# Kernel optimization log

Measured on AMD Instinct MI355X. Metric: run time of the kernel, lower is better.

## Reference

```python
import jax, jax.numpy as jnp
import numpy as np

T, B, IN, H, L = 300, 32, 320, 1024, 3  # seq, batch, input, hidden, layers (bidirectional)


def _init_params(key):
    stdv = 1.0 / np.sqrt(H)
    ks = jax.random.split(key, 8)
    u = lambda k, shp: jax.random.uniform(k, shp, jnp.float32, -stdv, stdv)
    # layer 0 (input IN), 2 directions
    w_ih0 = u(ks[0], (2, 4 * H, IN))
    w_hh0 = u(ks[1], (2, 4 * H, H))
    b_ih0 = u(ks[2], (2, 4 * H))
    b_hh0 = u(ks[3], (2, 4 * H))
    # layers 1..L-1 (input 2H), 2 directions
    w_ihL = u(ks[4], (L - 1, 2, 4 * H, 2 * H))
    w_hhL = u(ks[5], (L - 1, 2, 4 * H, H))
    b_ihL = u(ks[6], (L - 1, 2, 4 * H))
    b_hhL = u(ks[7], (L - 1, 2, 4 * H))
    # forget_gate_bias = 1.0 applied to bias_ih[H:2H], bias_hh[H:2H] = 0
    fgb = 1.0
    b_ih0 = b_ih0.at[:, H:2 * H].set(fgb)
    b_hh0 = b_hh0.at[:, H:2 * H].set(0.0)
    b_ihL = b_ihL.at[:, :, H:2 * H].set(fgb)
    b_hhL = b_hhL.at[:, :, H:2 * H].set(0.0)
    return dict(w_ih0=w_ih0, w_hh0=w_hh0, b_ih0=b_ih0, b_hh0=b_hh0,
                w_ihL=w_ihL, w_hhL=w_hhL, b_ihL=b_ihL, b_hhL=b_hhL)


def setup_inputs() -> dict:
    key = jax.random.key(0)
    k1, k2 = jax.random.split(key)
    inp = {
        "x": jax.random.normal(k1, (T, B, IN), jnp.float32),
        "h0": jnp.zeros((L * 2, B, H), jnp.float32),
        "c0": jnp.zeros((L * 2, B, H), jnp.float32),
    }
    inp.update(_init_params(k2))
    return inp


def _hard_sigmoid(z):
    return jnp.clip(0.2 * z + 0.5, 0.0, 1.0)


def _lstm_dir(x_seq, w_ih, w_hh, b_ih, b_hh, h0, c0, reverse):
    # x_seq: [T, B, D_in]; returns ys [T,B,H], (h,c) [B,H]
    xs = jnp.flip(x_seq, 0) if reverse else x_seq
    gx = jnp.einsum('tbi,gi->tbg', xs, w_ih) + b_ih + b_hh  # [T,B,4H]

    def step(carry, gxt):
        h, c = carry
        gates = gxt + h @ w_hh.T
        i, f, g, o = jnp.split(gates, 4, axis=-1)
        i = _hard_sigmoid(i)
        f = _hard_sigmoid(f)
        g = jnp.clip(g, -1.0, 1.0)  # hardtanh
        o = _hard_sigmoid(o)
        c = f * c + i * g
        h = o * jnp.clip(c, -1.0, 1.0)
        return (h, c), h

    (h, c), ys = jax.lax.scan(step, (h0, c0), gx)
    if reverse:
        ys = jnp.flip(ys, 0)
    return ys, h, c


def _stacked_forward(x, h0, c0, w_ih0, w_hh0, b_ih0, b_hh0, w_ihL, w_hhL, b_ihL, b_hhL):
    # Faithful to StackedLSTM: hn = hx[0].view(L,2,B,H); cn = hn (source bug: cell
    # init comes from h0, c0 ignored). h0/c0 are zeros so this is also correct math.
    hn = h0.reshape(L, 2, B, H)
    cn = hn
    out = x
    hs, cs = [], []
    for l in range(L):
        if l == 0:
            wih, whh, bih, bhh = w_ih0, w_hh0, b_ih0, b_hh0
        else:
            wih, whh, bih, bhh = w_ihL[l - 1], w_hhL[l - 1], b_ihL[l - 1], b_hhL[l - 1]
        yf, hf, cf = _lstm_dir(out, wih[0], whh[0], bih[0], bhh[0], hn[l, 0], cn[l, 0], False)
        yb, hb, cb = _lstm_dir(out, wih[1], whh[1], bih[1], bhh[1], hn[l, 1], cn[l, 1], True)
        out = jnp.concatenate([yf, yb], axis=-1)  # [T,B,2H]
        hs += [hf, hb]
        cs += [cf, cb]
    hn_out = jnp.stack(hs)  # [L*2, B, H]
    cn_out = jnp.stack(cs)
    return out, hn_out, cn_out


def reference(x, h0, c0, w_ih0, w_hh0, b_ih0, b_hh0, w_ihL, w_hhL, b_ihL, b_hhL):
    return _stacked_forward(x, h0, c0, w_ih0, w_hh0, b_ih0, b_hh0,
                            w_ihL, w_hhL, b_ihL, b_hhL)
```

## Files before the change

kernel.cpp:

```cpp
#include <hip/hip_runtime.h>

typedef __bf16 bf16;
typedef __attribute__((ext_vector_type(8))) __bf16 bf16x8;
typedef __attribute__((ext_vector_type(4))) float f32x4;

#define GLOBAL_AS __attribute__((address_space(1)))
#define LDS_AS __attribute__((address_space(3)))

__device__ __forceinline__ void gload_lds16(const void* g, void* l) {
  __builtin_amdgcn_global_load_lds((const GLOBAL_AS void*)g, (LDS_AS void*)l, 16, 0, 0);
}
__device__ __forceinline__ void gload_lds16_sc0(const void* g, void* l) {
  __builtin_amdgcn_global_load_lds((const GLOBAL_AS void*)g, (LDS_AS void*)l, 16, 0, 0x1);
}

__device__ __forceinline__ f32x4 mfma16(bf16x8 a, bf16x8 b, f32x4 c) {
  return __builtin_amdgcn_mfma_f32_16x16x32_bf16(a, b, c, 0, 0, 0);
}

#define GBAR() asm volatile("s_barrier" ::: "memory")

#define T_SEQ 300
#define NBATCH 32
#define DIN 320
#define NH 1024
#define NG 4096
#define MROWS 9600
#define OUT_Y 19660800
#define HN_SZ 196608
#define FPAD 32
#define ELEC_A (64 * FPAD)
#define ELEC_B (64 * FPAD + 8)
#define ELEC_R0 (64 * FPAD + 16)
#define ELEC_R1 (64 * FPAD + 24)
#define ELEC_G (64 * FPAD + 32)

__global__ __launch_bounds__(256) void k_cvt(const float* __restrict__ src,
                                             bf16* __restrict__ dst, int n8) {
  int stride = gridDim.x * blockDim.x;
  for (int i = blockIdx.x * blockDim.x + threadIdx.x; i < n8; i += stride) {
    const float* s = src + (size_t)i * 8;
    f32x4 a = *(const f32x4*)s;
    f32x4 b = *(const f32x4*)(s + 4);
    bf16x8 o;
#pragma unroll
    for (int j = 0; j < 4; ++j) { o[j] = (bf16)a[j]; o[j + 4] = (bf16)b[j]; }
    *(bf16x8*)(dst + (size_t)i * 8) = o;
  }
}

__global__ __launch_bounds__(256) void k_bsum(const float* __restrict__ bih0,
                                              const float* __restrict__ bhh0,
                                              const float* __restrict__ bihL,
                                              const float* __restrict__ bhhL,
                                              float* __restrict__ bsum) {
  int i = blockIdx.x * 256 + threadIdx.x;
  if (i < 2 * NG) bsum[i] = bih0[i] + bhh0[i];
  else            bsum[i] = bihL[i - 2 * NG] + bhhL[i - 2 * NG];
}

__global__ __launch_bounds__(256) void k_gemm_gx(const bf16* __restrict__ A,
                                                 const bf16* __restrict__ Bw,
                                                 const float* __restrict__ bias,
                                                 bf16* __restrict__ gxout, int K) {
  __shared__ bf16 As[128 * 32];
  __shared__ bf16 Bs[128 * 32];
  const int t = threadIdx.x;
  const int m0 = blockIdx.y * 128, n0 = blockIdx.x * 128;
  const int lane = t & 63, wid = t >> 6;
  const int wr = wid >> 1, wc = wid & 1;
  const int fr = lane & 15, fq = lane >> 4;
  f32x4 acc[4][4] = {};
  for (int k0 = 0; k0 < K; k0 += 32) {
#pragma unroll
    for (int r = 0; r < 2; ++r) {
      int idx = r * 256 + t;
      int row = idx >> 2, kk = (idx & 3) * 8;
      gload_lds16(A + (size_t)(m0 + row) * K + k0 + kk, As + (size_t)idx * 8);
      gload_lds16(Bw + (size_t)(n0 + row) * K + k0 + kk, Bs + (size_t)idx * 8);
    }
    asm volatile("s_waitcnt vmcnt(0)" ::: "memory");
    __syncthreads();
    bf16x8 af[4], bf_[4];
#pragma unroll
    for (int i2 = 0; i2 < 4; ++i2) {
      af[i2]  = *(const bf16x8*)(As + (wr * 64 + i2 * 16 + fr) * 32 + fq * 8);
      bf_[i2] = *(const bf16x8*)(Bs + (wc * 64 + i2 * 16 + fr) * 32 + fq * 8);
    }
#pragma unroll
    for (int mi = 0; mi < 4; ++mi)
#pragma unroll
      for (int ni = 0; ni < 4; ++ni)
        acc[mi][ni] = mfma16(af[mi], bf_[ni], acc[mi][ni]);
    __syncthreads();
  }
#pragma unroll
  for (int ni = 0; ni < 4; ++ni) {
    int col = n0 + wc * 64 + ni * 16 + fr;
    float bv = bias[col];
    int dir = col >> 12, grow = col & (NG - 1);
    int gg = grow >> 10, uu = grow & 1023;
    bf16* base = gxout + ((size_t)dir * 300 * 4 + gg) * 32768 + uu;
#pragma unroll
    for (int mi = 0; mi < 4; ++mi) {
#pragma unroll
      for (int j = 0; j < 4; ++j) {
        int row = m0 + wr * 64 + mi * 16 + fq * 4 + j;
        int tt = row >> 5, b = row & 31;
        base[(size_t)tt * 131072 + b * 1024] = (bf16)(acc[mi][ni][j] + bv);
      }
    }
  }
}

__global__ __launch_bounds__(256) void k_init(const float* __restrict__ h0,
                                              bf16* __restrict__ hbuf,
                                              int* __restrict__ flags, int layer) {
  int i = blockIdx.x * 256 + threadIdx.x;
  hbuf[i] = (bf16)h0[(size_t)layer * 65536 + i];
  if (blockIdx.x == 0) {
    for (int j = threadIdx.x; j < 64 * FPAD; j += 256) flags[j] = 0;
    if (threadIdx.x == 0) {
      flags[ELEC_A] = -1; flags[ELEC_B] = -1;
      flags[ELEC_R0] = 0; flags[ELEC_R1] = 0; flags[ELEC_G] = 0;
    }
  }
}

__global__ __launch_bounds__(512, 1) void k_rec(
    const bf16* __restrict__ whh,
    const bf16* __restrict__ gxT,
    const float* __restrict__ h0,
    bf16* __restrict__ hbuf,
    int* __restrict__ flags,
    bf16* __restrict__ yout,
    float* __restrict__ dout,
    int layer,
    const bf16* __restrict__ gB,
    const float* __restrict__ gbias,
    int ngemm) {
  __shared__ char smem_[131072];
  float* EX = (float*)smem_;
  char* GXL = smem_ + 67584;
  __shared__ int role2[2];

  const int tid = threadIdx.x;

  if (tid == 0) {
    int xcd;
    asm volatile("s_getreg_b32 %0, hwreg(HW_REG_XCC_ID)" : "=s"(xcd));
    xcd &= 0xf;
    int expct = -1;
    __hip_atomic_compare_exchange_strong(&flags[ELEC_A], &expct, xcd,
        __ATOMIC_ACQ_REL, __ATOMIC_RELAXED, __HIP_MEMORY_SCOPE_AGENT);
    int A;
    while ((A = __hip_atomic_load(&flags[ELEC_A], __ATOMIC_RELAXED,
                                  __HIP_MEMORY_SCOPE_AGENT)) == -1) {}
    int dir_ = -1;
    if (xcd == A) {
      dir_ = 0;
    } else {
      expct = -1;
      __hip_atomic_compare_exchange_strong(&flags[ELEC_B], &expct, xcd,
          __ATOMIC_ACQ_REL, __ATOMIC_RELAXED, __HIP_MEMORY_SCOPE_AGENT);
      int B;
      while ((B = __hip_atomic_load(&flags[ELEC_B], __ATOMIC_RELAXED,
                                    __HIP_MEMORY_SCOPE_AGENT)) == -1) {}
      if (xcd == B) dir_ = 1;
    }
    int rk;
    if (dir_ >= 0)
      rk = __hip_atomic_fetch_add(&flags[dir_ ? ELEC_R1 : ELEC_R0], 1,
                                  __ATOMIC_RELAXED, __HIP_MEMORY_SCOPE_AGENT);
    else
      rk = __hip_atomic_fetch_add(&flags[ELEC_G], 1,
                                  __ATOMIC_RELAXED, __HIP_MEMORY_SCOPE_AGENT);
    role2[0] = dir_; role2[1] = rk;
  }
  __syncthreads();
  const int dirx = role2[0];
  const int rankx = role2[1];

  if (dirx < 0) {
    const int gid = rankx;
    if (gid >= ngemm) return;
    const int lane = tid & 63, wid = tid >> 6;
    const int wm = wid >> 1, wn = wid & 1;
    const int fr = lane & 15, fq = lane >> 4;
    const int srow = tid >> 2;
    const int scol = (tid & 3) * 8;
    const int l16 = tid * 16;
#pragma unroll 1
    for (int i = 0; i < 7; ++i) {
      const int lin = i * 192 + gid;
      if (lin >= 1216) break;
      const int n0 = (lin & 31) << 8;
      const int mrank = lin >> 5;
      const int m = (mrank & 1) ? (19 + (mrank >> 1)) : (18 - (mrank >> 1));
      const int m0 = m << 8;
      int ra = 8 * m + 7; if (ra > 299) ra = 299;
      const int rb = 299 - 8 * m;
      const int thr = (ra > rb ? ra : rb) + 2;
      if (tid < 64) {
        while (__hip_atomic_load(&flags[tid * FPAD], __ATOMIC_RELAXED,
                                 __HIP_MEMORY_SCOPE_AGENT) < thr)
          __builtin_amdgcn_s_sleep(200);
      }
      __syncthreads();
      __builtin_amdgcn_fence(__ATOMIC_ACQUIRE, "agent");

      const bf16* ArowL = yout + (size_t)(m0 + srow) * 2048 + scol;
      const bf16* ArowH = yout + (size_t)(m0 + 128 + srow) * 2048 + scol;
      const bf16* BrowL = gB + (size_t)(n0 + srow) * 2048 + scol;
      const bf16* BrowH = gB + (size_t)(n0 + 128 + srow) * 2048 + scol;

      auto stage = [&](int ks) {
        char* buf = smem_ + (ks & 3) * 32768;
        gload_lds16(ArowL + ks * 32, buf + l16);
        gload_lds16(ArowH + ks * 32, buf + 8192 + l16);
        gload_lds16(BrowL + ks * 32, buf + 16384 + l16);
        gload_lds16(BrowH + ks * 32, buf + 24576 + l16);
      };

      f32x4 acc[4][8] = {};
      auto compute = [&](int k) {
        const bf16* As = (const bf16*)(smem_ + (k & 3) * 32768);
        const bf16* Bs = As + 8192;
        bf16x8 af[4], bfv[8];
#pragma unroll
        for (int i2 = 0; i2 < 4; ++i2)
          af[i2] = *(const bf16x8*)(As + (wm * 64 + i2 * 16 + fr) * 32 + fq * 8);
#pragma unroll
        for (int i2 = 0; i2 < 8; ++i2)
          bfv[i2] = *(const bf16x8*)(Bs + (wn * 128 + i2 * 16 + fr) * 32 + fq * 8);
#pragma unroll
        for (int mi = 0; mi < 4; ++mi)
#pragma unroll
          for (int ni = 0; ni < 8; ++ni)
            acc[mi][ni] = mfma16(af[mi], bfv[ni], acc[mi][ni]);
      };

      stage(0); stage(1); stage(2); stage(3);

#pragma unroll 1
      for (int k = 0; k < 60; ++k) {
        asm volatile("s_waitcnt vmcnt(12)" ::: "memory");
        GBAR();
        __builtin_amdgcn_sched_barrier(0);
        compute(k);
        __builtin_amdgcn_sched_barrier(0);
        GBAR();
        stage(k + 4);
      }
#define GTAIL(K, WAITS)                                          \
      asm volatile("s_waitcnt vmcnt(" WAITS ")" ::: "memory");   \
      GBAR();                                                    \
      __builtin_amdgcn_sched_barrier(0);                         \
      compute(K);                                                \
      __builtin_amdgcn_sched_barrier(0);                         \
      GBAR();
      GTAIL(60, "12") GTAIL(61, "8") GTAIL(62, "4") GTAIL(63, "0")
#undef GTAIL

#pragma unroll
      for (int ni = 0; ni < 8; ++ni) {
        int col = n0 + wn * 128 + ni * 16 + fr;
        float bv = gbias[col];
        int dirv = col >> 12, grow = col & (NG - 1);
        int gg = grow >> 10, uu = grow & 1023;
        bf16* base = (bf16*)gxT + ((size_t)dirv * 1200 + gg) * 32768 + uu;
#pragma unroll
        for (int mi = 0; mi < 4; ++mi) {
#pragma unroll
          for (int j = 0; j < 4; ++j) {
            int row = m0 + wm * 64 + mi * 16 + fq * 4 + j;
            if (row < MROWS) {
              int tt = row >> 5, b = row & 31;
              base[(size_t)tt * 131072 + b * 1024] = (bf16)(acc[mi][ni][j] + bv);
            }
          }
        }
      }
    }
    return;
  }

  const int dir = dirx;
  const int rank = rankx;
  const int u0 = rank << 5;
  const int w = tid >> 6, lane = tid & 63;
  const int fr = lane & 15, fq = lane >> 4;
  const int kh = w >> 1, rh = w & 1;
  const int fidx = (dir * 32 + rank) * FPAD;

  f32x4 wf[32];
#pragma unroll
  for (int rg = 0; rg < 4; ++rg) {
    int rowb = rh * 64 + rg * 16 + fr;
    const bf16* Wp = whh + ((size_t)dir * 4096 + (rowb >> 5) * 1024 + u0 + (rowb & 31)) * 1024
                     + kh * 256 + fq * 8;
#pragma unroll
    for (int it = 0; it < 8; ++it) wf[rg * 8 + it] = *(const f32x4*)(Wp + it * 32);
  }
#pragma unroll
  for (int i = 0; i < 32; ++i) asm volatile("" : "+v"(wf[i]));

  const int b_pt = tid >> 4;
  const int ul_pt = (tid & 15) << 1;
  const int ug_pt = u0 + ul_pt;
  const size_t soff = ((size_t)layer * 2 + dir) * 32768 + (size_t)b_pt * 1024 + ug_pt;
  float c0 = h0[soff], c1 = h0[soff + 1];
  float hl0 = 0.f, hl1 = 0.f;

  const int gg = tid >> 7, sub = tid & 127;
  const size_t gx_base0 = ((size_t)dir * 1200 + gg) * 32768
                          + (size_t)(sub >> 2) * 1024 + u0 + (sub & 3) * 8;

  int srcoff[8];
#pragma unroll
  for (int r = 0; r < 8; ++r) {
    int d = r * 8192 + tid * 16;
    int row = d >> 11, colb = d & 2047;
    srcoff[r] = row * 2048 + (colb ^ ((row & 7) << 4));
  }
  const int swz = (fr & 7) << 4;

  {
    const int ts0 = dir ? (T_SEQ - 1) : 0;
    gload_lds16(gxT + gx_base0 + (size_t)ts0 * 131072, GXL + tid * 16);
  }

#pragma unroll 1
  for (int t = 0; t < T_SEQ; ++t) {
    const int tseq = dir ? (T_SEQ - 1 - t) : t;

    if (tid < 32) {
      while (__hip_atomic_load(&flags[(dir * 32 + tid) * FPAD], __ATOMIC_RELAXED,
                               __HIP_MEMORY_SCOPE_AGENT) < t)
        __builtin_amdgcn_s_sleep(1);
    }
    __syncthreads();

    const char* hsrc = (const char*)hbuf + (((size_t)(t & 1) * 2 + dir) << 16);
#pragma unroll
    for (int r = 0; r < 8; ++r)
      gload_lds16_sc0(hsrc + srcoff[r], smem_ + r * 8192 + tid * 16);
    asm volatile("s_waitcnt vmcnt(0)" ::: "memory");
    __syncthreads();

    f32x4 acc[4][2] = {};
    const char* hb0 = smem_ + fr * 2048;
#pragma unroll
    for (int it = 0; it < 8; ++it) {
      int col = kh * 512 + it * 64 + fq * 16;
      bf16x8 ha0 = *(const bf16x8*)(hb0 + (col ^ swz));
      bf16x8 ha1 = *(const bf16x8*)(hb0 + 32768 + (col ^ swz));
#pragma unroll
      for (int rg = 0; rg < 4; ++rg) {
        bf16x8 wv = __builtin_bit_cast(bf16x8, wf[rg * 8 + it]);
        acc[rg][0] = mfma16(ha0, wv, acc[rg][0]);
        acc[rg][1] = mfma16(ha1, wv, acc[rg][1]);
      }
    }
    __syncthreads();

#pragma unroll
    for (int rg = 0; rg < 4; ++rg) {
      int rowb = rh * 64 + rg * 16 + fr;
      float* exr = EX + (size_t)(kh * 128 + rowb) * 33;
#pragma unroll
      for (int j = 0; j < 4; ++j) {
        exr[fq * 4 + j]      = acc[rg][0][j];
        exr[16 + fq * 4 + j] = acc[rg][1][j];
      }
    }
    __syncthreads();

    const bf16* gxb = (const bf16*)(GXL + (t & 1) * 8192);
    float hv[2]; float cc[2] = {c0, c1};
#pragma unroll
    for (int q = 0; q < 2; ++q) {
      int ul = ul_pt + q;
      float gt[4];
#pragma unroll
      for (int g2 = 0; g2 < 4; ++g2) {
        int rowb = g2 * 32 + ul;
        float s = EX[(size_t)(0 * 128 + rowb) * 33 + b_pt]
                + EX[(size_t)(1 * 128 + rowb) * 33 + b_pt]
                + EX[(size_t)(2 * 128 + rowb) * 33 + b_pt]
                + EX[(size_t)(3 * 128 + rowb) * 33 + b_pt];
        gt[g2] = s + (float)gxb[(g2 * 32 + b_pt) * 32 + ul];
      }
      float iv = fminf(fmaxf(__builtin_fmaf(0.2f, gt[0], 0.5f), 0.f), 1.f);
      float fv = fminf(fmaxf(__builtin_fmaf(0.2f, gt[1], 0.5f), 0.f), 1.f);
      float gv = fminf(fmaxf(gt[2], -1.f), 1.f);
      float ov = fminf(fmaxf(__builtin_fmaf(0.2f, gt[3], 0.5f), 0.f), 1.f);
      float c = fv * cc[q] + iv * gv;
      cc[q] = c;
      hv[q] = ov * fminf(fmaxf(c, -1.f), 1.f);
    }
    c0 = cc[0]; c1 = cc[1]; hl0 = hv[0]; hl1 = hv[1];

    unsigned hp;
    { union { bf16 h[2]; unsigned u; } pk; pk.h[0] = (bf16)hv[0]; pk.h[1] = (bf16)hv[1]; hp = pk.u; }
    {
      unsigned* hdst = (unsigned*)((char*)hbuf + (((size_t)((t + 1) & 1) * 2 + dir) << 16))
                       + (((size_t)b_pt * 1024 + ug_pt) >> 1);
      asm volatile("global_store_dword %0, %1, off" :: "v"(hdst), "v"(hp) : "memory");
    }
    asm volatile("s_waitcnt vmcnt(0)" ::: "memory");
    __syncthreads();
    if (tid == 0)
      __hip_atomic_store(&flags[fidx], t + 1, __ATOMIC_RELAXED, __HIP_MEMORY_SCOPE_AGENT);

    if (yout) {
      volatile unsigned* yd =
          (volatile unsigned*)((char*)yout
              + (((size_t)tseq * 32 + b_pt) * 2048 + dir * 1024 + ug_pt) * 2);
      *yd = hp;
    } else {
      float* yd = dout + ((size_t)tseq * 32 + b_pt) * 2048 + dir * 1024 + ug_pt;
      yd[0] = hv[0]; yd[1] = hv[1];
    }
    if (t + 1 < T_SEQ) {
      const int tn = dir ? (T_SEQ - 2 - t) : (t + 1);
      gload_lds16(gxT + gx_base0 + (size_t)tn * 131072,
                  GXL + ((t + 1) & 1) * 8192 + tid * 16);
    }
  }

  dout[OUT_Y + soff] = hl0;
  dout[OUT_Y + soff + 1] = hl1;
  dout[OUT_Y + HN_SZ + soff] = c0;
  dout[OUT_Y + HN_SZ + soff + 1] = c1;
  asm volatile("s_waitcnt vmcnt(0)" ::: "memory");
  __syncthreads();
  if (tid == 0)
    __hip_atomic_store(&flags[fidx], 302, __ATOMIC_RELAXED, __HIP_MEMORY_SCOPE_AGENT);
}

extern "C" void kernel_launch(void* const* d_in, const int* in_sizes, int n_in,
                              void* d_out, int out_size, void* d_ws, size_t ws_size,
                              hipStream_t stream) {
  const float* x     = (const float*)d_in[0];
  const float* h0    = (const float*)d_in[1];
  const float* w_ih0 = (const float*)d_in[3];
  const float* w_hh0 = (const float*)d_in[4];
  const float* b_ih0 = (const float*)d_in[5];
  const float* b_hh0 = (const float*)d_in[6];
  const float* w_ihL = (const float*)d_in[7];
  const float* w_hhL = (const float*)d_in[8];
  const float* b_ihL = (const float*)d_in[9];
  const float* b_hhL = (const float*)d_in[10];
  float* dout = (float*)d_out;
  char* ws = (char*)d_ws;

  const size_t OFF_XB   = 0;
  const size_t OFF_WIH0 = 6144000;
  const size_t OFF_WIHL = 11386880;
  const size_t OFF_WHH  = 78495744;
  const size_t OFF_BSUM = 128827392;
  const size_t OFF_GX   = 128925696;
  const size_t OFF_Y0   = 286212096;
  const size_t OFF_Y1   = 325533696;
  const size_t OFF_HBF  = 364855296;
  const size_t OFF_FLG  = 365117440;

  bf16*  xb    = (bf16*)(ws + OFF_XB);
  bf16*  wih0b = (bf16*)(ws + OFF_WIH0);
  bf16*  wihLb = (bf16*)(ws + OFF_WIHL);
  bf16*  whhb  = (bf16*)(ws + OFF_WHH);
  float* bsum  = (float*)(ws + OFF_BSUM);
  bf16*  gx    = (bf16*)(ws + OFF_GX);
  bf16*  y0    = (bf16*)(ws + OFF_Y0);
  bf16*  y1    = (bf16*)(ws + OFF_Y1);
  bf16*  hbuf  = (bf16*)(ws + OFF_HBF);
  int*   flags = (int*)(ws + OFF_FLG);

  auto cvt = [&](const float* s, bf16* d, size_t n) {
    int n8 = (int)(n / 8);
    int grid = (n8 + 255) / 256; if (grid > 2048) grid = 2048;
    k_cvt<<<grid, 256, 0, stream>>>(s, d, n8);
  };

  cvt(x,     xb,    (size_t)MROWS * DIN);
  cvt(w_ih0, wih0b, (size_t)2 * NG * DIN);
  cvt(w_ihL, wihLb, (size_t)2 * 2 * NG * 2048);
  cvt(w_hh0, whhb,  (size_t)2 * NG * NH);
  cvt(w_hhL, whhb + (size_t)2 * NG * NH, (size_t)4 * NG * NH);
  k_bsum<<<96, 256, 0, stream>>>(b_ih0, b_hh0, b_ihL, b_hhL, bsum);

  k_gemm_gx<<<dim3(64, 75), 256, 0, stream>>>(xb, wih0b, bsum, gx, DIN);

  for (int l = 0; l < 3; ++l) {
    k_init<<<256, 256, 0, stream>>>(h0, hbuf, flags, l);

    const bf16* whh_l = whhb + (size_t)l * 2 * NG * NH;
    bf16* yout = (l == 0) ? y0 : (l == 1 ? y1 : nullptr);
    const int ngemm = (l < 2) ? 192 : 0;
    const bf16* gB = wihLb + (size_t)l * 2 * NG * 2048;
    const float* gbias = bsum + (size_t)(l + 1) * 2 * NG;
    k_rec<<<256, 512, 0, stream>>>(whh_l, gx, h0, hbuf, flags, yout, dout, l,
                                   gB, gbias, ngemm);
  }
  (void)in_sizes; (void)n_in; (void)out_size; (void)ws_size;
}
```

Baseline: 3.894 ms.

## Use atomic tile queue for fused next-layer GEMM and let recurrence blocks join

```diff
diff --git a/kernel.cpp b/kernel.cpp
--- a/kernel.cpp
+++ b/kernel.cpp
@@ -34,6 +34,8 @@
 #define ELEC_R0 (64 * FPAD + 16)
 #define ELEC_R1 (64 * FPAD + 24)
 #define ELEC_G (64 * FPAD + 32)
+#define ELEC_T (64 * FPAD + 40)
+#define NTILES 1216
 
 __global__ __launch_bounds__(256) void k_cvt(const float* __restrict__ src,
                                              bf16* __restrict__ dst, int n8) {
@@ -123,6 +125,115 @@
     if (threadIdx.x == 0) {
       flags[ELEC_A] = -1; flags[ELEC_B] = -1;
       flags[ELEC_R0] = 0; flags[ELEC_R1] = 0; flags[ELEC_G] = 0;
+      flags[ELEC_T] = 0;
+    }
+  }
+}
+
+__device__ __forceinline__ void gemm_worker(
+    char* smem_, int* claimo, int tid, int* flags,
+    const bf16* __restrict__ yout, const bf16* __restrict__ gB,
+    const float* __restrict__ gbias, bf16* __restrict__ gxout) {
+  const int lane = tid & 63, wid = tid >> 6;
+  const int wm = wid >> 1, wn = wid & 1;
+  const int fr = lane & 15, fq = lane >> 4;
+  const int srow = tid >> 2;
+  const int scol = (tid & 3) * 8;
+  const int l16 = tid * 16;
+#pragma unroll 1
+  for (;;) {
+    if (tid == 0)
+      *claimo = __hip_atomic_fetch_add(&flags[ELEC_T], 1,
+                                       __ATOMIC_RELAXED, __HIP_MEMORY_SCOPE_AGENT);
+    __syncthreads();
+    const int lin = *claimo;
+    if (lin >= NTILES) return;
+    const int n0 = (lin & 31) << 8;
+    const int mrank = lin >> 5;
+    const int m = (mrank & 1) ? (19 + (mrank >> 1)) : (18 - (mrank >> 1));
+    const int m0 = m << 8;
+    int ra = 8 * m + 7; if (ra > 299) ra = 299;
+    const int rb = 299 - 8 * m;
+    const int thr = (ra > rb ? ra : rb) + 2;
+    if (tid < 64) {
+      while (__hip_atomic_load(&flags[tid * FPAD], __ATOMIC_RELAXED,
+                               __HIP_MEMORY_SCOPE_AGENT) < thr)
+        __builtin_amdgcn_s_sleep(200);
+    }
+    __syncthreads();
+    __builtin_amdgcn_fence(__ATOMIC_ACQUIRE, "agent");
+
+    const bf16* ArowL = yout + (size_t)(m0 + srow) * 2048 + scol;
+    const bf16* ArowH = yout + (size_t)(m0 + 128 + srow) * 2048 + scol;
+    const bf16* BrowL = gB + (size_t)(n0 + srow) * 2048 + scol;
+    const bf16* BrowH = gB + (size_t)(n0 + 128 + srow) * 2048 + scol;
+
+    auto stage = [&](int ks) {
+      char* buf = smem_ + (ks & 3) * 32768;
+      gload_lds16(ArowL + ks * 32, buf + l16);
+      gload_lds16(ArowH + ks * 32, buf + 8192 + l16);
+      gload_lds16(BrowL + ks * 32, buf + 16384 + l16);
+      gload_lds16(BrowH + ks * 32, buf + 24576 + l16);
+    };
+
+    f32x4 acc[4][8] = {};
+    auto compute = [&](int k) {
+      const bf16* As = (const bf16*)(smem_ + (k & 3) * 32768);
+      const bf16* Bs = As + 8192;
+      bf16x8 af[4], bfv[8];
+#pragma unroll
+      for (int i2 = 0; i2 < 4; ++i2)
+        af[i2] = *(const bf16x8*)(As + (wm * 64 + i2 * 16 + fr) * 32 + fq * 8);
+#pragma unroll
+      for (int i2 = 0; i2 < 8; ++i2)
+        bfv[i2] = *(const bf16x8*)(Bs + (wn * 128 + i2 * 16 + fr) * 32 + fq * 8);
+#pragma unroll
+      for (int mi = 0; mi < 4; ++mi)
+#pragma unroll
+        for (int ni = 0; ni < 8; ++ni)
+          acc[mi][ni] = mfma16(af[mi], bfv[ni], acc[mi][ni]);
+    };
+
+    stage(0); stage(1); stage(2); stage(3);
+
+#pragma unroll 1
+    for (int k = 0; k < 60; ++k) {
+      asm volatile("s_waitcnt vmcnt(12)" ::: "memory");
+      GBAR();
+      __builtin_amdgcn_sched_barrier(0);
+      compute(k);
+      __builtin_amdgcn_sched_barrier(0);
+      GBAR();
+      stage(k + 4);
+    }
+#define GTAIL(K, WAITS)                                          \
+    asm volatile("s_waitcnt vmcnt(" WAITS ")" ::: "memory");     \
+    GBAR();                                                      \
+    __builtin_amdgcn_sched_barrier(0);                           \
+    compute(K);                                                  \
+    __builtin_amdgcn_sched_barrier(0);                           \
+    GBAR();
+    GTAIL(60, "12") GTAIL(61, "8") GTAIL(62, "4") GTAIL(63, "0")
+#undef GTAIL
+
+#pragma unroll
+    for (int ni = 0; ni < 8; ++ni) {
+      int col = n0 + wn * 128 + ni * 16 + fr;
+      float bv = gbias[col];
+      int dirv = col >> 12, grow = col & (NG - 1);
+      int gg = grow >> 10, uu = grow & 1023;
+      bf16* base = gxout + ((size_t)dirv * 1200 + gg) * 32768 + uu;
+#pragma unroll
+      for (int mi = 0; mi < 4; ++mi) {
+#pragma unroll
+        for (int j = 0; j < 4; ++j) {
+          int row = m0 + wm * 64 + mi * 16 + fq * 4 + j;
+          if (row < MROWS) {
+            int tt = row >> 5, b = row & 31;
+            base[(size_t)tt * 131072 + b * 1024] = (bf16)(acc[mi][ni][j] + bv);
+          }
+        }
+      }
     }
   }
 }
@@ -143,6 +254,7 @@
   float* EX = (float*)smem_;
   char* GXL = smem_ + 67584;
   __shared__ int role2[2];
+  __shared__ int claimo;
 
   const int tid = threadIdx.x;
 
@@ -168,13 +280,10 @@
                                     __HIP_MEMORY_SCOPE_AGENT)) == -1) {}
       if (xcd == B) dir_ = 1;
     }
-    int rk;
+    int rk = 0;
     if (dir_ >= 0)
       rk = __hip_atomic_fetch_add(&flags[dir_ ? ELEC_R1 : ELEC_R0], 1,
                                   __ATOMIC_RELAXED, __HIP_MEMORY_SCOPE_AGENT);
-    else
-      rk = __hip_atomic_fetch_add(&flags[ELEC_G], 1,
-                                  __ATOMIC_RELAXED, __HIP_MEMORY_SCOPE_AGENT);
     role2[0] = dir_; role2[1] = rk;
   }
   __syncthreads();
@@ -182,106 +291,8 @@
   const int rankx = role2[1];
 
   if (dirx < 0) {
-    const int gid = rankx;
-    if (gid >= ngemm) return;
-    const int lane = tid & 63, wid = tid >> 6;
-    const int wm = wid >> 1, wn = wid & 1;
-    const int fr = lane & 15, fq = lane >> 4;
-    const int srow = tid >> 2;
-    const int scol = (tid & 3) * 8;
-    const int l16 = tid * 16;
-#pragma unroll 1
-    for (int i = 0; i < 7; ++i) {
-      const int lin = i * 192 + gid;
-      if (lin >= 1216) break;
-      const int n0 = (lin & 31) << 8;
-      const int mrank = lin >> 5;
-      const int m = (mrank & 1) ? (19 + (mrank >> 1)) : (18 - (mrank >> 1));
-      const int m0 = m << 8;
-      int ra = 8 * m + 7; if (ra > 299) ra = 299;
-      const int rb = 299 - 8 * m;
-      const int thr = (ra > rb ? ra : rb) + 2;
-      if (tid < 64) {
-        while (__hip_atomic_load(&flags[tid * FPAD], __ATOMIC_RELAXED,
-                                 __HIP_MEMORY_SCOPE_AGENT) < thr)
-          __builtin_amdgcn_s_sleep(200);
-      }
-      __syncthreads();
-      __builtin_amdgcn_fence(__ATOMIC_ACQUIRE, "agent");
-
-      const bf16* ArowL = yout + (size_t)(m0 + srow) * 2048 + scol;
-      const bf16* ArowH = yout + (size_t)(m0 + 128 + srow) * 2048 + scol;
-      const bf16* BrowL = gB + (size_t)(n0 + srow) * 2048 + scol;
-      const bf16* BrowH = gB + (size_t)(n0 + 128 + srow) * 2048 + scol;
-
-      auto stage = [&](int ks) {
-        char* buf = smem_ + (ks & 3) * 32768;
-        gload_lds16(ArowL + ks * 32, buf + l16);
-        gload_lds16(ArowH + ks * 32, buf + 8192 + l16);
-        gload_lds16(BrowL + ks * 32, buf + 16384 + l16);
-        gload_lds16(BrowH + ks * 32, buf + 24576 + l16);
-      };
-
-      f32x4 acc[4][8] = {};
-      auto compute = [&](int k) {
-        const bf16* As = (const bf16*)(smem_ + (k & 3) * 32768);
-        const bf16* Bs = As + 8192;
-        bf16x8 af[4], bfv[8];
-#pragma unroll
-        for (int i2 = 0; i2 < 4; ++i2)
-          af[i2] = *(const bf16x8*)(As + (wm * 64 + i2 * 16 + fr) * 32 + fq * 8);
-#pragma unroll
-        for (int i2 = 0; i2 < 8; ++i2)
-          bfv[i2] = *(const bf16x8*)(Bs + (wn * 128 + i2 * 16 + fr) * 32 + fq * 8);
-#pragma unroll
-        for (int mi = 0; mi < 4; ++mi)
-#pragma unroll
-          for (int ni = 0; ni < 8; ++ni)
-            acc[mi][ni] = mfma16(af[mi], bfv[ni], acc[mi][ni]);
-      };
-
-      stage(0); stage(1); stage(2); stage(3);
-
-#pragma unroll 1
-      for (int k = 0; k < 60; ++k) {
-        asm volatile("s_waitcnt vmcnt(12)" ::: "memory");
-        GBAR();
-        __builtin_amdgcn_sched_barrier(0);
-        compute(k);
-        __builtin_amdgcn_sched_barrier(0);
-        GBAR();
-        stage(k + 4);
-      }
-#define GTAIL(K, WAITS)                                          \
-      asm volatile("s_waitcnt vmcnt(" WAITS ")" ::: "memory");   \
-      GBAR();                                                    \
-      __builtin_amdgcn_sched_barrier(0);                         \
-      compute(K);                                                \
-      __builtin_amdgcn_sched_barrier(0);                         \
-      GBAR();
-      GTAIL(60, "12") GTAIL(61, "8") GTAIL(62, "4") GTAIL(63, "0")
-#undef GTAIL
-
-#pragma unroll
-      for (int ni = 0; ni < 8; ++ni) {
-        int col = n0 + wn * 128 + ni * 16 + fr;
-        float bv = gbias[col];
-        int dirv = col >> 12, grow = col & (NG - 1);
-        int gg = grow >> 10, uu = grow & 1023;
-        bf16* base = (bf16*)gxT + ((size_t)dirv * 1200 + gg) * 32768 + uu;
-#pragma unroll
-        for (int mi = 0; mi < 4; ++mi) {
-#pragma unroll
-          for (int j = 0; j < 4; ++j) {
-            int row = m0 + wm * 64 + mi * 16 + fq * 4 + j;
-            if (row < MROWS) {
-              int tt = row >> 5, b = row & 31;
-              base[(size_t)tt * 131072 + b * 1024] = (bf16)(acc[mi][ni][j] + bv);
-            }
-          }
-        }
-      }
-    }
+    if (ngemm > 0)
+      gemm_worker(smem_, &claimo, tid, flags, yout, gB, gbias, (bf16*)gxT);
     return;
   }
 
@@ -437,6 +448,9 @@
   __syncthreads();
   if (tid == 0)
     __hip_atomic_store(&flags[fidx], 302, __ATOMIC_RELAXED, __HIP_MEMORY_SCOPE_AGENT);
+
+  if (ngemm > 0)
+    gemm_worker(smem_, &claimo, tid, flags, yout, gB, gbias, (bf16*)gxT);
 }
 
 extern "C" void kernel_launch(void* const* d_in, const int* in_sizes, int n_in,
```

Measured after the change: 3.827 ms. Within noise of the previous version (-1.7%).
